# Optimization experiments

Measured on AMD Instinct MI355X. Metric: run time of the kernel, lower is better.

Reference implementation:

```python
import jax, jax.numpy as jnp
import numpy as np

N_NODES = 100000
N_GRAPHS = 128

def _graph_conv(x, W, b, s, d, n_nodes):
    """DGL GraphConv with norm='both': D_dst^{-1/2} A D_src^{-1/2} X W + b."""
    ones = jnp.ones(s.shape[0], x.dtype)
    deg_out = jax.ops.segment_sum(ones, s, num_segments=n_nodes)  # src out-degree
    deg_in = jax.ops.segment_sum(ones, d, num_segments=n_nodes)   # dst in-degree
    norm_src = jnp.where(deg_out > 0, 1.0 / jnp.sqrt(jnp.maximum(deg_out, 1.0)), 0.0)
    norm_dst = jnp.where(deg_in > 0, 1.0 / jnp.sqrt(jnp.maximum(deg_in, 1.0)), 0.0)
    h = x * norm_src[:, None]                    # [N, F]
    agg = jax.ops.segment_sum(h[s], d, num_segments=n_nodes)  # SpMM gather-scatter
    rst = (agg @ W) * norm_dst[:, None] + b
    return rst

def _hetero_layer(x, Ws, bs, src, dst, n_nodes):
    # HeteroGraphConv aggregate='sum' over relations (fixed small set -> loop ok)
    out = jnp.zeros((n_nodes, Ws.shape[-1]), x.dtype)
    for r in range(Ws.shape[0]):
        out = out + _graph_conv(x, Ws[r], bs[r], src[r], dst[r], n_nodes)
    return out

def setup_inputs() -> dict:
    key = jax.random.key(0)
    ks = jax.random.split(key, 8)
    feat = jax.random.normal(ks[0], (N_NODES, 256), dtype=jnp.float32)
    src = jax.random.randint(ks[1], (3, 400000), 0, N_NODES)
    dst = jax.random.randint(ks[2], (3, 400000), 0, N_NODES)
    graph_ids = jnp.sort(jax.random.randint(ks[3], (N_NODES,), 0, N_GRAPHS))
    W1 = jax.random.normal(ks[4], (3, 256, 256), dtype=jnp.float32) * 0.06
    b1 = jnp.zeros((3, 256), dtype=jnp.float32)
    W2 = jax.random.normal(ks[5], (3, 256, 256), dtype=jnp.float32) * 0.06
    b2 = jnp.zeros((3, 256), dtype=jnp.float32)
    return {"feat": feat, "src": src, "dst": dst, "graph_ids": graph_ids,
            "W1": W1, "b1": b1, "W2": W2, "b2": b2}

def reference(feat, src, dst, graph_ids, W1, b1, W2, b2):
    n_nodes = feat.shape[0]
    h = _hetero_layer(feat, W1, b1, src, dst, n_nodes)
    h = jax.nn.relu(h)
    h = _hetero_layer(h, W2, b2, src, dst, n_nodes)
    # AvgPooling over batched graphs
    sums = jax.ops.segment_sum(h, graph_ids, num_segments=N_GRAPHS)
    counts = jax.ops.segment_sum(jnp.ones(n_nodes, h.dtype), graph_ids, num_segments=N_GRAPHS)
    return sums / jnp.maximum(counts, 1.0)[:, None]
```

## Files before the change

kernel.cpp:

```cpp
#include <hip/hip_runtime.h>
#include <stdint.h>

#define NN 100000
#define NE 400000
#define NR 3
#define NF 256
#define NK 768
#define NG 128
#define SCAN_NB ((NN + 1023) / 1024)

typedef __attribute__((ext_vector_type(4))) unsigned short ushortx4;
typedef __attribute__((ext_vector_type(8))) unsigned short ushortx8;
typedef __attribute__((ext_vector_type(8))) short short8;
typedef __attribute__((ext_vector_type(4))) float floatx4;

static __device__ __forceinline__ unsigned short f2bfu(float f) {
  union { float f; uint32_t u; } c; c.f = f;
  uint32_t x = c.u;
  uint32_t r = (x + 0x7fffu + ((x >> 16) & 1u)) >> 16;
  return (unsigned short)r;
}
static __device__ __forceinline__ float bfu2f(unsigned short u) {
  union { uint32_t u; float f; } c; c.u = ((uint32_t)u) << 16;
  return c.f;
}

static __device__ __forceinline__ void gload16(const void* g, void* l) {
  __builtin_amdgcn_global_load_lds(
      (const __attribute__((address_space(1))) uint32_t*)g,
      (__attribute__((address_space(3))) uint32_t*)l, 16, 0, 0);
}


__global__ __launch_bounds__(256) void degree_kernel(
    const int* __restrict__ src, const int* __restrict__ dst,
    int* __restrict__ deg_out, int* __restrict__ deg_in) {
  int t = blockIdx.x * 256 + threadIdx.x;
  int r = blockIdx.y;
  if (t < NE) {
    atomicAdd(&deg_out[r * NN + src[r * NE + t]], 1);
    atomicAdd(&deg_in[r * NN + dst[r * NE + t]], 1);
  }
}

__global__ __launch_bounds__(128) void gcount_kernel(
    const int* __restrict__ gid, int* __restrict__ gcount) {
  int g = threadIdx.x;
  int lo = 0, hi = NN;
  while (lo < hi) { int mid = (lo + hi) >> 1; if (gid[mid] < g) lo = mid + 1; else hi = mid; }
  int a = lo;
  lo = 0; hi = NN;
  while (lo < hi) { int mid = (lo + hi) >> 1; if (gid[mid] < g + 1) lo = mid + 1; else hi = mid; }
  gcount[g] = lo - a;
}

__global__ __launch_bounds__(256) void norm_kernel(
    const int* __restrict__ deg_out, const int* __restrict__ deg_in,
    float* __restrict__ n_src, float* __restrict__ n_dst) {
  int t = blockIdx.x * 256 + threadIdx.x;
  if (t < NR * NN) {
    int dof = deg_out[t], din = deg_in[t];
    n_src[t] = dof > 0 ? rsqrtf((float)dof) : 0.f;
    n_dst[t] = din > 0 ? rsqrtf((float)din) : 0.f;
  }
}


__global__ __launch_bounds__(256) void scan_phaseA(
    const int* __restrict__ deg_in, int* __restrict__ blocksum) {
  int r = blockIdx.y, b = blockIdx.x, tid = threadIdx.x;
  const int* deg = deg_in + (size_t)r * NN;
  int base = b * 1024 + tid * 4;
  int s = 0;
#pragma unroll
  for (int i = 0; i < 4; ++i) { int idx = base + i; if (idx < NN) s += deg[idx]; }
  __shared__ int red[256];
  red[tid] = s; __syncthreads();
  for (int off = 128; off > 0; off >>= 1) {
    if (tid < off) red[tid] += red[tid + off];
    __syncthreads();
  }
  if (tid == 0) blocksum[r * SCAN_NB + b] = red[0];
}

__global__ __launch_bounds__(128) void scan_phaseB(
    int* __restrict__ blocksum, int* __restrict__ rowptr) {
  int r = blockIdx.x, tid = threadIdx.x;
  int* bs = blocksum + r * SCAN_NB;
  __shared__ int buf[128];
  int v = (tid < SCAN_NB) ? bs[tid] : 0;
  buf[tid] = v; __syncthreads();
  for (int off = 1; off < 128; off <<= 1) {
    int t = (tid >= off) ? buf[tid - off] : 0;
    __syncthreads();
    buf[tid] += t;
    __syncthreads();
  }
  if (tid < SCAN_NB) bs[tid] = buf[tid] - v;
  if (tid == 127) rowptr[(size_t)r * (NN + 1) + NN] = buf[127];
}

__global__ __launch_bounds__(256) void scan_phaseC(
    const int* __restrict__ deg_in, const int* __restrict__ blocksum,
    int* __restrict__ rowptr) {
  int r = blockIdx.y, b = blockIdx.x, tid = threadIdx.x;
  const int* deg = deg_in + (size_t)r * NN;
  int* rp = rowptr + (size_t)r * (NN + 1);
  int base = b * 1024 + tid * 4;
  int v[4]; int s = 0;
#pragma unroll
  for (int i = 0; i < 4; ++i) { int idx = base + i; v[i] = (idx < NN) ? deg[idx] : 0; s += v[i]; }
  __shared__ int buf[256];
  buf[tid] = s; __syncthreads();
  for (int off = 1; off < 256; off <<= 1) {
    int t = (tid >= off) ? buf[tid - off] : 0;
    __syncthreads();
    buf[tid] += t;
    __syncthreads();
  }
  int excl = buf[tid] - s + blocksum[r * SCAN_NB + b];
#pragma unroll
  for (int i = 0; i < 4; ++i) {
    int idx = base + i;
    if (idx < NN) rp[idx] = excl;
    excl += v[i];
  }
}

__global__ __launch_bounds__(256) void scatter_kernel(
    const int* __restrict__ src, const int* __restrict__ dst,
    int* __restrict__ cursor, const float* __restrict__ n_src,
    int2* __restrict__ csr_e) {
  int t = blockIdx.x * 256 + threadIdx.x;
  int r = blockIdx.y;
  if (t < NE) {
    int s = src[r * NE + t], v = dst[r * NE + t];
    int pos = atomicAdd(&cursor[r * (NN + 1) + v], 1);
    csr_e[(size_t)r * NE + pos] = make_int2(s, __float_as_int(n_src[r * NN + s]));
  }
}


__global__ __launch_bounds__(256) void prep_w_kernel(
    const float* __restrict__ W1, const float* __restrict__ W2,
    unsigned short* __restrict__ wt1, unsigned short* __restrict__ wt2) {
  int t = blockIdx.x * 256 + threadIdx.x;
  int lay = t / (NR * NF * NF);
  int rem = t % (NR * NF * NF);
  int r = rem / (NF * NF);
  int k = (rem / NF) % NF;
  int n = rem % NF;
  const float* W = lay ? W2 : W1;
  unsigned short* wt = lay ? wt2 : wt1;
  wt[(size_t)n * NK + r * NF + k] = f2bfu(W[((size_t)r * NF + k) * NF + n]);
}

__global__ __launch_bounds__(256) void prep_bias_kernel(
    const float* __restrict__ b1, const float* __restrict__ b2,
    float* __restrict__ bs1, float* __restrict__ bs2) {
  int t = blockIdx.x * 256 + threadIdx.x;
  if (t < 2 * NF) {
    int lay = t / NF, n = t % NF;
    const float* b = lay ? b2 : b1;
    float* bs = lay ? bs2 : bs1;
    bs[n] = b[n] + b[NF + n] + b[2 * NF + n];
  }
}

__global__ __launch_bounds__(256) void cast_kernel(
    const float* __restrict__ in, unsigned short* __restrict__ out, int n4) {
  int t = blockIdx.x * 256 + threadIdx.x;
  if (t < n4) {
    floatx4 v = *(const floatx4*)&in[(size_t)t * 4];
    ushortx4 o;
    o.x = f2bfu(v.x); o.y = f2bfu(v.y); o.z = f2bfu(v.z); o.w = f2bfu(v.w);
    *(ushortx4*)&out[(size_t)t * 4] = o;
  }
}


__global__ __launch_bounds__(256) void spmm_kernel(
    const unsigned short* __restrict__ x,
    const int* __restrict__ rowptr, const int2* __restrict__ csr_e,
    const float* __restrict__ n_dst,
    unsigned short* __restrict__ agg) {
  int wid = threadIdx.x >> 6, l = threadIdx.x & 63;
  int v = blockIdx.x * 4 + wid;
  if (v >= NN) return;
  const int half = l >> 5;
  const int c8 = (l & 31) * 8;

  int ea = rowptr[v],                e1a = rowptr[v + 1];
  int eb = rowptr[(NN + 1) + v],     e1b = rowptr[(NN + 1) + v + 1];
  int ec = rowptr[2 * (NN + 1) + v], e1c = rowptr[2 * (NN + 1) + v + 1];
  const int2* cea = csr_e;
  const int2* ceb = csr_e + (size_t)NE;
  const int2* cec = csr_e + (size_t)2 * NE;

  float a[NR][8];
#pragma unroll
  for (int r = 0; r < NR; ++r)
#pragma unroll
    for (int j = 0; j < 8; ++j) a[r][j] = 0.f;

  while (ea < e1a || eb < e1b || ec < e1c) {
    if (ea < e1a) {
      if (ea + half < e1a) {
        int2 p = cea[ea + half];
        float w = __int_as_float(p.y);
        ushortx8 xv = *(const ushortx8*)&x[(size_t)p.x * NF + c8];
#pragma unroll
        for (int j = 0; j < 8; ++j) a[0][j] += w * bfu2f(xv[j]);
      }
      ea += 2;
    }
    if (eb < e1b) {
      if (eb + half < e1b) {
        int2 p = ceb[eb + half];
        float w = __int_as_float(p.y);
        ushortx8 xv = *(const ushortx8*)&x[(size_t)p.x * NF + c8];
#pragma unroll
        for (int j = 0; j < 8; ++j) a[1][j] += w * bfu2f(xv[j]);
      }
      eb += 2;
    }
    if (ec < e1c) {
      if (ec + half < e1c) {
        int2 p = cec[ec + half];
        float w = __int_as_float(p.y);
        ushortx8 xv = *(const ushortx8*)&x[(size_t)p.x * NF + c8];
#pragma unroll
        for (int j = 0; j < 8; ++j) a[2][j] += w * bfu2f(xv[j]);
      }
      ec += 2;
    }
  }

#pragma unroll
  for (int r = 0; r < NR; ++r)
#pragma unroll
    for (int j = 0; j < 8; ++j) a[r][j] += __shfl_xor(a[r][j], 32);

  if (l < 32) {
#pragma unroll
    for (int r = 0; r < NR; ++r) {
      float nd = n_dst[r * NN + v];
      ushortx8 o;
#pragma unroll
      for (int j = 0; j < 8; ++j) o[j] = f2bfu(a[r][j] * nd);
      *(ushortx8*)&agg[(size_t)v * NK + r * NF + c8] = o;
    }
  }
}


__global__ __launch_bounds__(256, 2) void gemm_kernel(
    const unsigned short* __restrict__ A,
    const unsigned short* __restrict__ Bt,
    const float* __restrict__ bias,
    unsigned short* __restrict__ C,
    int M, int relu) {
  __shared__ unsigned short ldsA[128 * 32];
  __shared__ unsigned short ldsB[256 * 32];
  const int tid = threadIdx.x;
  const int l = tid & 63, wid = tid >> 6;
  const int row0 = blockIdx.x * 128;
  const int c0 = wid * 64;

  floatx4 acc[8][4];
#pragma unroll
  for (int i = 0; i < 8; ++i)
#pragma unroll
    for (int j = 0; j < 4; ++j)
#pragma unroll
      for (int q = 0; q < 4; ++q) acc[i][j][q] = 0.f;

  const int fr = l & 15, fk = (l >> 4) * 8;

  for (int kt = 0; kt < NK / 32; ++kt) {
    const int k0 = kt * 32;
    {
      int u = wid * 64 + l;
      int arow = row0 + (u >> 2);
      if (arow >= M) arow = M - 1;
      gload16(A + (size_t)arow * NK + k0 + (u & 3) * 8, &ldsA[u * 8]);
      u += 256;
      arow = row0 + (u >> 2);
      if (arow >= M) arow = M - 1;
      gload16(A + (size_t)arow * NK + k0 + (u & 3) * 8, &ldsA[u * 8]);
    }
#pragma unroll
    for (int p = 0; p < 4; ++p) {
      int u = p * 256 + wid * 64 + l;
      int col = u >> 2;
      gload16(Bt + (size_t)col * NK + k0 + (u & 3) * 8, &ldsB[u * 8]);
    }
    asm volatile("s_waitcnt vmcnt(0)" ::: "memory");
    __syncthreads();

    short8 af[8], bf[4];
#pragma unroll
    for (int m = 0; m < 8; ++m)
      af[m] = *(const short8*)&ldsA[(m * 16 + fr) * 32 + fk];
#pragma unroll
    for (int n = 0; n < 4; ++n)
      bf[n] = *(const short8*)&ldsB[(c0 + n * 16 + fr) * 32 + fk];
#pragma unroll
    for (int m = 0; m < 8; ++m)
#pragma unroll
      for (int n = 0; n < 4; ++n)
        acc[m][n] = __builtin_amdgcn_mfma_f32_16x16x32_bf16(af[m], bf[n], acc[m][n], 0, 0, 0);
    __syncthreads();
  }

  const int fq = l >> 4;
#pragma unroll
  for (int m = 0; m < 8; ++m) {
#pragma unroll
    for (int n = 0; n < 4; ++n) {
      int col = c0 + n * 16 + fr;
      float bv = bias[col];
#pragma unroll
      for (int q = 0; q < 4; ++q) {
        int row = row0 + m * 16 + fq * 4 + q;
        if (row < M) {
          float vv = acc[m][n][q] + bv;
          if (relu) vv = fmaxf(vv, 0.f);
          C[(size_t)row * NF + col] = f2bfu(vv);
        }
      }
    }
  }
}


__global__ __launch_bounds__(256) void pool_kernel(
    const unsigned short* __restrict__ h2, const int* __restrict__ gid,
    float* __restrict__ poolsum) {
  int c = threadIdx.x;
  int v0 = blockIdx.x * 256;
  int vend = min(v0 + 256, NN);
  float acc = 0.f;
  int curg = -1;
  for (int v = v0; v < vend; ++v) {
    int g = gid[v];
    if (g != curg) {
      if (curg >= 0) atomicAdd(&poolsum[curg * NF + c], acc);
      curg = g; acc = 0.f;
    }
    acc += bfu2f(h2[(size_t)v * NF + c]);
  }
  if (curg >= 0) atomicAdd(&poolsum[curg * NF + c], acc);
}

__global__ __launch_bounds__(256) void final_kernel(
    const float* __restrict__ poolsum, const int* __restrict__ gcount,
    float* __restrict__ out) {
  int g = blockIdx.x, c = threadIdx.x;
  out[g * NF + c] = poolsum[g * NF + c] / fmaxf((float)gcount[g], 1.f);
}


extern "C" void kernel_launch(void* const* d_in, const int* in_sizes, int n_in,
                              void* d_out, int out_size, void* d_ws, size_t ws_size,
                              hipStream_t stream) {
  const float* feat = (const float*)d_in[0];
  const int* src = (const int*)d_in[1];
  const int* dst = (const int*)d_in[2];
  const int* gid = (const int*)d_in[3];
  const float* W1 = (const float*)d_in[4];
  const float* b1 = (const float*)d_in[5];
  const float* W2 = (const float*)d_in[6];
  const float* b2 = (const float*)d_in[7];
  float* out = (float*)d_out;

  char* ws = (char*)d_ws;
  size_t off = 0;
  auto alloc = [&](size_t bytes) -> void* {
    void* p = ws + off;
    off = (off + bytes + 255) & ~(size_t)255;
    return p;
  };

  int* deg_out = (int*)alloc((size_t)NR * NN * 4);
  int* deg_in  = (int*)alloc((size_t)NR * NN * 4);
  float* poolsum = (float*)alloc((size_t)NG * NF * 4);
  size_t zero_bytes = off;

  int* cursor  = (int*)alloc((size_t)NR * (NN + 1) * 4);
  int* gcount  = (int*)alloc((size_t)NG * 4);
  int* blocksum = (int*)alloc((size_t)NR * SCAN_NB * 4);
  float* n_src = (float*)alloc((size_t)NR * NN * 4);
  float* n_dst = (float*)alloc((size_t)NR * NN * 4);
  int* rowptr  = (int*)alloc((size_t)NR * (NN + 1) * 4);
  int2* csr_e  = (int2*)alloc((size_t)NR * NE * 8);
  unsigned short* wt1 = (unsigned short*)alloc((size_t)NF * NK * 2);
  unsigned short* wt2 = (unsigned short*)alloc((size_t)NF * NK * 2);
  float* bs1 = (float*)alloc(NF * 4);
  float* bs2 = (float*)alloc(NF * 4);
  unsigned short* featbf = (unsigned short*)alloc((size_t)NN * NF * 2);
  unsigned short* h1 = (unsigned short*)alloc((size_t)NN * NF * 2);
  unsigned short* h2 = (unsigned short*)alloc((size_t)NN * NF * 2);
  unsigned short* agg = (unsigned short*)alloc((size_t)NN * NK * 2);
  (void)ws_size; (void)in_sizes; (void)n_in; (void)out_size;

  hipMemsetAsync(d_ws, 0, zero_bytes, stream);

  dim3 eg((NE + 255) / 256, NR);
  degree_kernel<<<eg, 256, 0, stream>>>(src, dst, deg_out, deg_in);
  gcount_kernel<<<1, 128, 0, stream>>>(gid, gcount);
  norm_kernel<<<(NR * NN + 255) / 256, 256, 0, stream>>>(deg_out, deg_in, n_src, n_dst);
  scan_phaseA<<<dim3(SCAN_NB, NR), 256, 0, stream>>>(deg_in, blocksum);
  scan_phaseB<<<NR, 128, 0, stream>>>(blocksum, rowptr);
  scan_phaseC<<<dim3(SCAN_NB, NR), 256, 0, stream>>>(deg_in, blocksum, rowptr);
  hipMemcpyAsync(cursor, rowptr, (size_t)NR * (NN + 1) * 4,
                 hipMemcpyDeviceToDevice, stream);
  scatter_kernel<<<eg, 256, 0, stream>>>(src, dst, cursor, n_src, csr_e);

  prep_w_kernel<<<(2 * NR * NF * NF) / 256, 256, 0, stream>>>(W1, W2, wt1, wt2);
  prep_bias_kernel<<<2, 256, 0, stream>>>(b1, b2, bs1, bs2);
  cast_kernel<<<(NN * NF / 4 + 255) / 256, 256, 0, stream>>>(feat, featbf, NN * NF / 4);

  spmm_kernel<<<(NN + 3) / 4, 256, 0, stream>>>(featbf, rowptr, csr_e, n_dst, agg);
  gemm_kernel<<<(NN + 127) / 128, 256, 0, stream>>>(agg, wt1, bs1, h1, NN, 1);
  spmm_kernel<<<(NN + 3) / 4, 256, 0, stream>>>(h1, rowptr, csr_e, n_dst, agg);
  gemm_kernel<<<(NN + 127) / 128, 256, 0, stream>>>(agg, wt2, bs2, h2, NN, 0);
  pool_kernel<<<(NN + 255) / 256, 256, 0, stream>>>(h2, gid, poolsum);
  final_kernel<<<NG, 256, 0, stream>>>(poolsum, gcount, out);
}
```

Before: 713.2 us.

## Double-buffer GEMM LDS tiles and add nontemporal loads/stores in cast and SpMM

The GEMM kernel now uses two LDS buffers and issues the global-to-LDS loads for the next K tile before running the MFMAs on the current one, so memory latency overlaps with compute and one barrier per iteration goes away. The cast kernel input load and the SpMM output store become nontemporal to reduce cache pollution on streaming data. Double buffering doubles LDS use to 48KB per block, which may limit how many blocks can be resident at the requested 2 per CU.

```diff
diff --git a/kernel.cpp b/kernel.cpp
--- a/kernel.cpp
+++ b/kernel.cpp
@@ -171,7 +171,7 @@
     const float* __restrict__ in, unsigned short* __restrict__ out, int n4) {
   int t = blockIdx.x * 256 + threadIdx.x;
   if (t < n4) {
-    floatx4 v = *(const floatx4*)&in[(size_t)t * 4];
+    floatx4 v = __builtin_nontemporal_load((const floatx4*)&in[(size_t)t * 4]);
     ushortx4 o;
     o.x = f2bfu(v.x); o.y = f2bfu(v.y); o.z = f2bfu(v.z); o.w = f2bfu(v.w);
     *(ushortx4*)&out[(size_t)t * 4] = o;
@@ -248,7 +248,7 @@
       ushortx8 o;
 #pragma unroll
       for (int j = 0; j < 8; ++j) o[j] = f2bfu(a[r][j] * nd);
-      *(ushortx8*)&agg[(size_t)v * NK + r * NF + c8] = o;
+      __builtin_nontemporal_store(o, (ushortx8*)&agg[(size_t)v * NK + r * NF + c8]);
     }
   }
 }
@@ -260,8 +260,8 @@
     const float* __restrict__ bias,
     unsigned short* __restrict__ C,
     int M, int relu) {
-  __shared__ unsigned short ldsA[128 * 32];
-  __shared__ unsigned short ldsB[256 * 32];
+  __shared__ unsigned short ldsA[2][128 * 32];
+  __shared__ unsigned short ldsB[2][256 * 32];
   const int tid = threadIdx.x;
   const int l = tid & 63, wid = tid >> 6;
   const int row0 = blockIdx.x * 128;
@@ -277,40 +277,47 @@
 
   const int fr = l & 15, fk = (l >> 4) * 8;
 
+  auto stage = [&](int b, int kt) {
+    const int k0 = kt * 32;
+    int u = wid * 64 + l;
+    int arow = row0 + (u >> 2);
+    if (arow >= M) arow = M - 1;
+    gload16(A + (size_t)arow * NK + k0 + (u & 3) * 8, &ldsA[b][u * 8]);
+    u += 256;
+    arow = row0 + (u >> 2);
+    if (arow >= M) arow = M - 1;
+    gload16(A + (size_t)arow * NK + k0 + (u & 3) * 8, &ldsA[b][u * 8]);
+#pragma unroll
+    for (int p = 0; p < 4; ++p) {
+      int uu = p * 256 + wid * 64 + l;
+      gload16(Bt + (size_t)(uu >> 2) * NK + k0 + (uu & 3) * 8, &ldsB[b][uu * 8]);
+    }
+  };
+
+  stage(0, 0);
+  asm volatile("s_waitcnt vmcnt(0)" ::: "memory");
+  __syncthreads();
+
+  int cur = 0;
   for (int kt = 0; kt < NK / 32; ++kt) {
-    const int k0 = kt * 32;
-    {
-      int u = wid * 64 + l;
-      int arow = row0 + (u >> 2);
-      if (arow >= M) arow = M - 1;
-      gload16(A + (size_t)arow * NK + k0 + (u & 3) * 8, &ldsA[u * 8]);
-      u += 256;
-      arow = row0 + (u >> 2);
-      if (arow >= M) arow = M - 1;
-      gload16(A + (size_t)arow * NK + k0 + (u & 3) * 8, &ldsA[u * 8]);
-    }
-#pragma unroll
-    for (int p = 0; p < 4; ++p) {
-      int u = p * 256 + wid * 64 + l;
-      int col = u >> 2;
-      gload16(Bt + (size_t)col * NK + k0 + (u & 3) * 8, &ldsB[u * 8]);
-    }
-    asm volatile("s_waitcnt vmcnt(0)" ::: "memory");
-    __syncthreads();
+    if (kt + 1 < NK / 32) stage(cur ^ 1, kt + 1);
 
     short8 af[8], bf[4];
 #pragma unroll
     for (int m = 0; m < 8; ++m)
-      af[m] = *(const short8*)&ldsA[(m * 16 + fr) * 32 + fk];
+      af[m] = *(const short8*)&ldsA[cur][(m * 16 + fr) * 32 + fk];
 #pragma unroll
     for (int n = 0; n < 4; ++n)
-      bf[n] = *(const short8*)&ldsB[(c0 + n * 16 + fr) * 32 + fk];
+      bf[n] = *(const short8*)&ldsB[cur][(c0 + n * 16 + fr) * 32 + fk];
 #pragma unroll
     for (int m = 0; m < 8; ++m)
 #pragma unroll
       for (int n = 0; n < 4; ++n)
         acc[m][n] = __builtin_amdgcn_mfma_f32_16x16x32_bf16(af[m], bf[n], acc[m][n], 0, 0, 0);
-    __syncthreads();
+
+    asm volatile("s_waitcnt vmcnt(0)" ::: "memory");
+    __syncthreads();
+    cur ^= 1;
   }
 
   const int fq = l >> 4;
```

New measurement: 711.0 us. No clear change (-0.3%).

## Fuse SpMM aggregation with GEMM via LDS-resident swizzled aggregate tile

Applied to the files above, without the earlier changes.

Merges the sparse aggregation and dense weight GEMM into one kernel. Each block aggregates 32 destination rows into a swizzled shared-memory tile, then multiplies it by the transposed weights with MFMA, reading B directly from global memory. This removes the round trip of the 100000x768 bf16 aggregate buffer through HBM and one launch per layer. In exchange B is re-read per block without LDS staging, and the GEMM tile is smaller. The cast kernel also switches to nontemporal loads.

```diff
diff --git a/kernel.cpp b/kernel.cpp
--- a/kernel.cpp
+++ b/kernel.cpp
@@ -8,6 +8,7 @@
 #define NK 768
 #define NG 128
 #define SCAN_NB ((NN + 1023) / 1024)
+#define BMF 32
 
 typedef __attribute__((ext_vector_type(4))) unsigned short ushortx4;
 typedef __attribute__((ext_vector_type(8))) unsigned short ushortx8;
@@ -23,12 +24,6 @@
 static __device__ __forceinline__ float bfu2f(unsigned short u) {
   union { uint32_t u; float f; } c; c.u = ((uint32_t)u) << 16;
   return c.f;
-}
-
-static __device__ __forceinline__ void gload16(const void* g, void* l) {
-  __builtin_amdgcn_global_load_lds(
-      (const __attribute__((address_space(1))) uint32_t*)g,
-      (__attribute__((address_space(3))) uint32_t*)l, 16, 0, 0);
 }
 
 
@@ -171,7 +166,7 @@
     const float* __restrict__ in, unsigned short* __restrict__ out, int n4) {
   int t = blockIdx.x * 256 + threadIdx.x;
   if (t < n4) {
-    floatx4 v = *(const floatx4*)&in[(size_t)t * 4];
+    floatx4 v = __builtin_nontemporal_load((const floatx4*)&in[(size_t)t * 4]);
     ushortx4 o;
     o.x = f2bfu(v.x); o.y = f2bfu(v.y); o.z = f2bfu(v.z); o.w = f2bfu(v.w);
     *(ushortx4*)&out[(size_t)t * 4] = o;
@@ -179,155 +174,136 @@
 }
 
 
-__global__ __launch_bounds__(256) void spmm_kernel(
+__global__ __launch_bounds__(256, 3) void fused_kernel(
     const unsigned short* __restrict__ x,
     const int* __restrict__ rowptr, const int2* __restrict__ csr_e,
     const float* __restrict__ n_dst,
-    unsigned short* __restrict__ agg) {
-  int wid = threadIdx.x >> 6, l = threadIdx.x & 63;
-  int v = blockIdx.x * 4 + wid;
-  if (v >= NN) return;
+    const unsigned short* __restrict__ Bt,
+    const float* __restrict__ bias,
+    unsigned short* __restrict__ out,
+    int relu) {
+  __shared__ __align__(16) unsigned short aggl[BMF][NK];
+  char* aggb = (char*)&aggl[0][0];
+  const int wid = threadIdx.x >> 6, l = threadIdx.x & 63;
   const int half = l >> 5;
   const int c8 = (l & 31) * 8;
 
-  int ea = rowptr[v],                e1a = rowptr[v + 1];
-  int eb = rowptr[(NN + 1) + v],     e1b = rowptr[(NN + 1) + v + 1];
-  int ec = rowptr[2 * (NN + 1) + v], e1c = rowptr[2 * (NN + 1) + v + 1];
-  const int2* cea = csr_e;
-  const int2* ceb = csr_e + (size_t)NE;
-  const int2* cec = csr_e + (size_t)2 * NE;
-
-  float a[NR][8];
-#pragma unroll
-  for (int r = 0; r < NR; ++r)
-#pragma unroll
-    for (int j = 0; j < 8; ++j) a[r][j] = 0.f;
-
-  while (ea < e1a || eb < e1b || ec < e1c) {
-    if (ea < e1a) {
-      if (ea + half < e1a) {
-        int2 p = cea[ea + half];
-        float w = __int_as_float(p.y);
-        ushortx8 xv = *(const ushortx8*)&x[(size_t)p.x * NF + c8];
-#pragma unroll
-        for (int j = 0; j < 8; ++j) a[0][j] += w * bfu2f(xv[j]);
+  for (int i = 0; i < 8; ++i) {
+    const int vi = i * 4 + wid;
+    const int v = blockIdx.x * BMF + vi;
+
+    int ea = rowptr[v],                e1a = rowptr[v + 1];
+    int eb = rowptr[(NN + 1) + v],     e1b = rowptr[(NN + 1) + v + 1];
+    int ec = rowptr[2 * (NN + 1) + v], e1c = rowptr[2 * (NN + 1) + v + 1];
+    const int2* cea = csr_e;
+    const int2* ceb = csr_e + (size_t)NE;
+    const int2* cec = csr_e + (size_t)2 * NE;
+
+    float a[NR][8];
+#pragma unroll
+    for (int r = 0; r < NR; ++r)
+#pragma unroll
+      for (int j = 0; j < 8; ++j) a[r][j] = 0.f;
+
+    while (ea < e1a || eb < e1b || ec < e1c) {
+      if (ea < e1a) {
+        if (ea + half < e1a) {
+          int2 p = cea[ea + half];
+          float w = __int_as_float(p.y);
+          ushortx8 xv = *(const ushortx8*)&x[(size_t)p.x * NF + c8];
+#pragma unroll
+          for (int j = 0; j < 8; ++j) a[0][j] += w * bfu2f(xv[j]);
+        }
+        ea += 2;
       }
-      ea += 2;
-    }
-    if (eb < e1b) {
-      if (eb + half < e1b) {
-        int2 p = ceb[eb + half];
-        float w = __int_as_float(p.y);
-        ushortx8 xv = *(const ushortx8*)&x[(size_t)p.x * NF + c8];
-#pragma unroll
-        for (int j = 0; j < 8; ++j) a[1][j] += w * bfu2f(xv[j]);
+      if (eb < e1b) {
+        if (eb + half < e1b) {
+          int2 p = ceb[eb + half];
+          float w = __int_as_float(p.y);
+          ushortx8 xv = *(const ushortx8*)&x[(size_t)p.x * NF + c8];
+#pragma unroll
+          for (int j = 0; j < 8; ++j) a[1][j] += w * bfu2f(xv[j]);
+        }
+        eb += 2;
       }
-      eb += 2;
-    }
-    if (ec < e1c) {
-      if (ec + half < e1c) {
-        int2 p = cec[ec + half];
-        float w = __int_as_float(p.y);
-        ushortx8 xv = *(const ushortx8*)&x[(size_t)p.x * NF + c8];
-#pragma unroll
-        for (int j = 0; j < 8; ++j) a[2][j] += w * bfu2f(xv[j]);
+      if (ec < e1c) {
+        if (ec + half < e1c) {
+          int2 p = cec[ec + half];
+          float w = __int_as_float(p.y);
+          ushortx8 xv = *(const ushortx8*)&x[(size_t)p.x * NF + c8];
+#pragma unroll
+          for (int j = 0; j < 8; ++j) a[2][j] += w * bfu2f(xv[j]);
+        }
+        ec += 2;
       }
-      ec += 2;
-    }
-  }
-
-#pragma unroll
-  for (int r = 0; r < NR; ++r)
-#pragma unroll
-    for (int j = 0; j < 8; ++j) a[r][j] += __shfl_xor(a[r][j], 32);
-
-  if (l < 32) {
-#pragma unroll
-    for (int r = 0; r < NR; ++r) {
-      float nd = n_dst[r * NN + v];
-      ushortx8 o;
-#pragma unroll
-      for (int j = 0; j < 8; ++j) o[j] = f2bfu(a[r][j] * nd);
-      *(ushortx8*)&agg[(size_t)v * NK + r * NF + c8] = o;
-    }
-  }
-}
-
-
-__global__ __launch_bounds__(256, 2) void gemm_kernel(
-    const unsigned short* __restrict__ A,
-    const unsigned short* __restrict__ Bt,
-    const float* __restrict__ bias,
-    unsigned short* __restrict__ C,
-    int M, int relu) {
-  __shared__ unsigned short ldsA[128 * 32];
-  __shared__ unsigned short ldsB[256 * 32];
-  const int tid = threadIdx.x;
-  const int l = tid & 63, wid = tid >> 6;
-  const int row0 = blockIdx.x * 128;
+    }
+
+#pragma unroll
+    for (int r = 0; r < NR; ++r)
+#pragma unroll
+      for (int j = 0; j < 8; ++j) a[r][j] += __shfl_xor(a[r][j], 32);
+
+    if (l < 32) {
+      const int rowbyte = vi * (NK * 2);
+      const int sw = (vi & 7) << 4;
+#pragma unroll
+      for (int r = 0; r < NR; ++r) {
+        float nd = n_dst[r * NN + v];
+        ushortx8 o;
+#pragma unroll
+        for (int j = 0; j < 8; ++j) o[j] = f2bfu(a[r][j] * nd);
+        int colbyte = (r * NF + c8) * 2;
+        *(ushortx8*)(aggb + rowbyte + (colbyte ^ sw)) = o;
+      }
+    }
+  }
+  __syncthreads();
+
   const int c0 = wid * 64;
-
-  floatx4 acc[8][4];
-#pragma unroll
-  for (int i = 0; i < 8; ++i)
-#pragma unroll
-    for (int j = 0; j < 4; ++j)
-#pragma unroll
-      for (int q = 0; q < 4; ++q) acc[i][j][q] = 0.f;
-
-  const int fr = l & 15, fk = (l >> 4) * 8;
-
+  const int fr = l & 15, fkb = (l >> 4) * 16;
+
+  floatx4 acc[2][4];
+#pragma unroll
+  for (int m = 0; m < 2; ++m)
+#pragma unroll
+    for (int n = 0; n < 4; ++n)
+#pragma unroll
+      for (int q = 0; q < 4; ++q) acc[m][n][q] = 0.f;
+
+#pragma unroll 2
   for (int kt = 0; kt < NK / 32; ++kt) {
-    const int k0 = kt * 32;
-    {
-      int u = wid * 64 + l;
-      int arow = row0 + (u >> 2);
-      if (arow >= M) arow = M - 1;
-      gload16(A + (size_t)arow * NK + k0 + (u & 3) * 8, &ldsA[u * 8]);
-      u += 256;
-      arow = row0 + (u >> 2);
-      if (arow >= M) arow = M - 1;
-      gload16(A + (size_t)arow * NK + k0 + (u & 3) * 8, &ldsA[u * 8]);
-    }
-#pragma unroll
-    for (int p = 0; p < 4; ++p) {
-      int u = p * 256 + wid * 64 + l;
-      int col = u >> 2;
-      gload16(Bt + (size_t)col * NK + k0 + (u & 3) * 8, &ldsB[u * 8]);
-    }
-    asm volatile("s_waitcnt vmcnt(0)" ::: "memory");
-    __syncthreads();
-
-    short8 af[8], bf[4];
-#pragma unroll
-    for (int m = 0; m < 8; ++m)
-      af[m] = *(const short8*)&ldsA[(m * 16 + fr) * 32 + fk];
-#pragma unroll
-    for (int n = 0; n < 4; ++n)
-      bf[n] = *(const short8*)&ldsB[(c0 + n * 16 + fr) * 32 + fk];
-#pragma unroll
-    for (int m = 0; m < 8; ++m)
+    const int kb = kt * 64;
+    short8 af[2], bf[4];
+#pragma unroll
+    for (int m = 0; m < 2; ++m) {
+      int row = m * 16 + fr;
+      af[m] = *(const short8*)(aggb + row * (NK * 2) + ((kb + fkb) ^ ((row & 7) << 4)));
+    }
+#pragma unroll
+    for (int n = 0; n < 4; ++n) {
+      int col = c0 + n * 16 + fr;
+      bf[n] = *(const short8*)((const char*)Bt + (size_t)col * (NK * 2) + kb + fkb);
+    }
+#pragma unroll
+    for (int m = 0; m < 2; ++m)
 #pragma unroll
       for (int n = 0; n < 4; ++n)
         acc[m][n] = __builtin_amdgcn_mfma_f32_16x16x32_bf16(af[m], bf[n], acc[m][n], 0, 0, 0);
-    __syncthreads();
   }
 
   const int fq = l >> 4;
 #pragma unroll
-  for (int m = 0; m < 8; ++m) {
+  for (int m = 0; m < 2; ++m) {
 #pragma unroll
     for (int n = 0; n < 4; ++n) {
       int col = c0 + n * 16 + fr;
       float bv = bias[col];
 #pragma unroll
       for (int q = 0; q < 4; ++q) {
-        int row = row0 + m * 16 + fq * 4 + q;
-        if (row < M) {
-          float vv = acc[m][n][q] + bv;
-          if (relu) vv = fmaxf(vv, 0.f);
-          C[(size_t)row * NF + col] = f2bfu(vv);
-        }
+        int row = blockIdx.x * BMF + m * 16 + fq * 4 + q;
+        float vv = acc[m][n][q] + bv;
+        if (relu) vv = fmaxf(vv, 0.f);
+        out[(size_t)row * NF + col] = f2bfu(vv);
       }
     }
   }
@@ -401,7 +377,6 @@
   unsigned short* featbf = (unsigned short*)alloc((size_t)NN * NF * 2);
   unsigned short* h1 = (unsigned short*)alloc((size_t)NN * NF * 2);
   unsigned short* h2 = (unsigned short*)alloc((size_t)NN * NF * 2);
-  unsigned short* agg = (unsigned short*)alloc((size_t)NN * NK * 2);
   (void)ws_size; (void)in_sizes; (void)n_in; (void)out_size;
 
   hipMemsetAsync(d_ws, 0, zero_bytes, stream);
@@ -421,10 +396,10 @@
   prep_bias_kernel<<<2, 256, 0, stream>>>(b1, b2, bs1, bs2);
   cast_kernel<<<(NN * NF / 4 + 255) / 256, 256, 0, stream>>>(feat, featbf, NN * NF / 4);
 
-  spmm_kernel<<<(NN + 3) / 4, 256, 0, stream>>>(featbf, rowptr, csr_e, n_dst, agg);
-  gemm_kernel<<<(NN + 127) / 128, 256, 0, stream>>>(agg, wt1, bs1, h1, NN, 1);
-  spmm_kernel<<<(NN + 3) / 4, 256, 0, stream>>>(h1, rowptr, csr_e, n_dst, agg);
-  gemm_kernel<<<(NN + 127) / 128, 256, 0, stream>>>(agg, wt2, bs2, h2, NN, 0);
+  fused_kernel<<<NN / BMF, 256, 0, stream>>>(featbf, rowptr, csr_e, n_dst,
+                                             wt1, bs1, h1, 1);
+  fused_kernel<<<NN / BMF, 256, 0, stream>>>(h1, rowptr, csr_e, n_dst,
+                                             wt2, bs2, h2, 0);
   pool_kernel<<<(NN + 255) / 256, 256, 0, stream>>>(h2, gid, poolsum);
   final_kernel<<<NG, 256, 0, stream>>>(poolsum, gcount, out);
 }
```

After: 977.3 us. +37.0%, slower.
